# Kernel optimization log

Hardware: AMD Instinct MI355X
Metric: run time of the kernel (lower is better)

Reference implementation:

```python
import jax, jax.numpy as jnp
import numpy as np

LN_EPS = 1e-5  # torch.nn.LayerNorm default


def setup_inputs() -> dict:
    key = jax.random.key(0)
    k1, k2 = jax.random.split(key)
    C = 64
    x = jax.random.normal(k1, (1, C, 64, 96, 96), dtype=jnp.float32)
    ln_gamma = jnp.ones((C,), jnp.float32)
    ln_beta = jnp.zeros((C,), jnp.float32)
    # Conv3d(C, 3C, 1, groups=C) -> per-channel scalar weight [3C] and bias [3C]
    conv_w = jax.random.normal(k2, (3 * C,), dtype=jnp.float32) * 0.02
    conv_b = jnp.zeros((3 * C,), jnp.float32)
    return {"x": x, "ln_gamma": ln_gamma, "ln_beta": ln_beta,
            "conv_w": conv_w, "conv_b": conv_b}


def reference(x, ln_gamma, ln_beta, conv_w, conv_b):
    B, C, D, H, W = x.shape
    N = D * H * W
    xf = x.reshape(B, C, N)  # [B, C, N]

    # LayerNorm over the channel dim (module permutes channels last)
    mean = jnp.mean(xf, axis=1, keepdims=True)
    var = jnp.mean(jnp.square(xf - mean), axis=1, keepdims=True)
    y = (xf - mean) * jax.lax.rsqrt(var + LN_EPS)
    y = y * ln_gamma[None, :, None] + ln_beta[None, :, None]

    # grouped 1x1x1 conv: output channel o reads input channel o // 3
    idx = jnp.arange(3 * C) // 3
    y3 = y[:, idx, :] * conv_w[None, :, None] + conv_b[None, :, None]  # [B, 3C, N]
    q, k, v = jnp.split(y3, 3, axis=1)  # each [B, C, N]

    # channel (cross-covariance) attention: logits [B, C, C]
    logits = jnp.einsum('bcn,bkn->bck', q, k) * (C ** -0.5)
    attn = jax.nn.softmax(logits, axis=-1)  # max-subtraction built in
    out = jnp.einsum('bck,bkn->bcn', attn, v).reshape(B, C, D, H, W)
    return x + out
```

## Files before the change

kernel.cpp:

```cpp
#include <hip/hip_runtime.h>

#define NPOS 589824
#define LN_EPS 1e-5f

typedef _Float16 half8 __attribute__((ext_vector_type(8)));
typedef _Float16 half2_t __attribute__((ext_vector_type(2)));
typedef float f32x4 __attribute__((ext_vector_type(4)));
typedef float f32x2 __attribute__((ext_vector_type(2)));

static __device__ __forceinline__ half2_t pk16(float a, float b) {
    return __builtin_bit_cast(half2_t, __builtin_amdgcn_cvt_pkrtz(a, b));
}

#define KB_BLOCKS 1152
#define YSTR 520


__global__ __launch_bounds__(256) void csa_stats(
    const float* __restrict__ x, float* __restrict__ stats)
{
    const int g = blockIdx.x * 256 + threadIdx.x;
    const f32x4* __restrict__ x4 = (const f32x4*)x;
    f32x4 s = {0.f,0.f,0.f,0.f}, sq = s;
    #pragma unroll
    for (int c = 0; c < 64; ++c) {
        f32x4 v = x4[(size_t)c * (NPOS/4) + g];
        s += v;
        sq += v * v;
    }
    const f32x4 mu = s * (1.f/64.f);
    const f32x4 var = sq * (1.f/64.f) - mu * mu;
    f32x4 o0, o1;
    o0[0] = mu[0]; o0[2] = mu[1]; o1[0] = mu[2]; o1[2] = mu[3];
    o0[1] = rsqrtf(fmaxf(var[0], 0.f) + LN_EPS);
    o0[3] = rsqrtf(fmaxf(var[1], 0.f) + LN_EPS);
    o1[1] = rsqrtf(fmaxf(var[2], 0.f) + LN_EPS);
    o1[3] = rsqrtf(fmaxf(var[3], 0.f) + LN_EPS);
    f32x4* st4 = (f32x4*)stats;
    st4[2*g]     = o0;
    st4[2*g + 1] = o1;
}

__global__ __launch_bounds__(256, 3) void csa_gram(
    const float* __restrict__ x, const float* __restrict__ lng,
    const float* __restrict__ lnb, const float* __restrict__ stats,
    float* __restrict__ partials)
{
    __shared__ __align__(16) _Float16 Y[45][YSTR];
    const int tid = threadIdx.x;
    const int lane = tid & 63;
    const int wv = tid >> 6;

    for (int i = tid; i < YSTR; i += 256) {
        Y[43][i] = (_Float16)1.0f;
        Y[44][i] = (_Float16)0.0f;
    }

    const int t = blockIdx.x * 256 + tid;
    const f32x4 st = ((const f32x4*)stats)[t];
    const float mu0 = st[0], rin0 = st[1], mu1 = st[2], rin1 = st[3];
    const int n0 = t * 2;
    #pragma unroll
    for (int c = 0; c < 43; ++c) {
        f32x2 v = *(const f32x2*)(x + (size_t)c * NPOS + n0);
        const float g = lng[c], b = lnb[c];
        const float y0 = fmaf((v[0] - mu0) * rin0, g, b);
        const float y1 = fmaf((v[1] - mu1) * rin1, g, b);
        *(half2_t*)&Y[c][tid * 2] = pk16(y0, y1);
    }
    __syncthreads();

    f32x4 acc00 = {0.f,0.f,0.f,0.f}, acc01 = acc00, acc10 = acc00, acc11 = acc00;
    const int row = lane & 15;
    const int sub = (lane >> 4) & 3;
    const int kbase = wv * 128 + sub * 8;
    const int r16 = row + 16;
    const int ra1 = (r16 < 22) ? r16 : ((r16 == 22) ? 43 : 44);
    const int rb1 = (r16 < 22) ? (r16 + 21) : ((r16 == 22) ? 43 : 44);
    #pragma unroll
    for (int s2 = 0; s2 < 4; ++s2) {
        const int kk = kbase + s2 * 32;
        half8 a0 = *(const half8*)&Y[row][kk];
        half8 a1 = *(const half8*)&Y[ra1][kk];
        half8 b0 = *(const half8*)&Y[row + 21][kk];
        half8 b1 = *(const half8*)&Y[rb1][kk];
        acc00 = __builtin_amdgcn_mfma_f32_16x16x32_f16(a0, b0, acc00, 0, 0, 0);
        acc01 = __builtin_amdgcn_mfma_f32_16x16x32_f16(a0, b1, acc01, 0, 0, 0);
        acc10 = __builtin_amdgcn_mfma_f32_16x16x32_f16(a1, b0, acc10, 0, 0, 0);
        acc11 = __builtin_amdgcn_mfma_f32_16x16x32_f16(a1, b1, acc11, 0, 0, 0);
    }
    __syncthreads();

    float* G32 = (float*)&Y[0][0];
    for (int e = tid; e < 1024; e += 256) G32[e] = 0.f;
    __syncthreads();
    const int r0 = (lane >> 4) * 4, c0 = lane & 15;
    #pragma unroll
    for (int r = 0; r < 4; ++r) {
        atomicAdd(&G32[(r0 + r) * 32 + c0],            acc00[r]);
        atomicAdd(&G32[(r0 + r) * 32 + 16 + c0],       acc01[r]);
        atomicAdd(&G32[(16 + r0 + r) * 32 + c0],       acc10[r]);
        atomicAdd(&G32[(16 + r0 + r) * 32 + 16 + c0],  acc11[r]);
    }
    __syncthreads();
    for (int e = tid; e < 576; e += 256) {
        const int r = e / 24, c = e % 24;
        partials[(size_t)blockIdx.x * 576 + e] = G32[r * 32 + c];
    }
}

__global__ __launch_bounds__(256) void csa_k2(const float* __restrict__ partials,
                                              float* __restrict__ gfin)
{
    const int tid = threadIdx.x;
    const int e = blockIdx.x * 16 + (tid >> 4);
    const int g = tid & 15;
    float s = 0.f;
    for (int b = g; b < KB_BLOCKS; b += 16)
        s += partials[(size_t)b * 576 + e];
    s += __shfl_down(s, 8, 16);
    s += __shfl_down(s, 4, 16);
    s += __shfl_down(s, 2, 16);
    s += __shfl_down(s, 1, 16);
    if (g == 0) gfin[e] = s;
}

__global__ void csa_k3(const float* __restrict__ G, const float* __restrict__ cw,
                       const float* __restrict__ cb, float* __restrict__ M,
                       float* __restrict__ betaO)
{
    const int c = threadIdx.x;
    __shared__ float lg[64][65];
    const float wq = cw[c], bq = cb[c];
    const int a = c / 3;
    const float Sa = G[a * 24 + 22];
    float mx = -1e30f;
    #pragma unroll
    for (int k = 0; k < 64; ++k) {
        const float wk = cw[64 + k], bk = cb[64 + k];
        const int b = (64 + k) / 3 - 21;
        const float Gab = G[a * 24 + b];
        const float Sb  = G[22 * 24 + b];
        float lo = 0.125f * (wq * wk * Gab + wq * bk * Sa + bq * wk * Sb
                             + bq * bk * (float)NPOS);
        lg[c][k] = lo;
        mx = fmaxf(mx, lo);
    }
    float sum = 0.f;
    #pragma unroll
    for (int k = 0; k < 64; ++k) {
        float e = expf(lg[c][k] - mx);
        lg[c][k] = e; sum += e;
    }
    const float inv = 1.f / sum;
    float Ml[22];
    #pragma unroll
    for (int m = 0; m < 22; ++m) Ml[m] = 0.f;
    float bacc = 0.f;
    #pragma unroll
    for (int k = 0; k < 64; ++k) {
        const float attn = lg[c][k] * inv;
        const int mm = (128 + k) / 3 - 42;
        Ml[mm] = fmaf(attn, cw[128 + k], Ml[mm]);
        bacc   = fmaf(attn, cb[128 + k], bacc);
    }
    #pragma unroll
    for (int m = 0; m < 22; ++m) M[c * 22 + m] = Ml[m];
    betaO[c] = bacc;
}

__global__ __launch_bounds__(256, 2) void csa_k4(
    const float* __restrict__ x, const float* __restrict__ lng,
    const float* __restrict__ lnb, const float* __restrict__ M,
    const float* __restrict__ betaO, float* __restrict__ out)
{
    const int n0 = (blockIdx.x * 256 + threadIdx.x) * 2;
    f32x2 xv[64];
    f32x2 s = {0.f, 0.f}, sq = s;
    #pragma unroll
    for (int c = 0; c < 64; ++c) {
        f32x2 v = *(const f32x2*)(x + (size_t)c * NPOS + n0);
        xv[c] = v; s += v; sq += v * v;
    }
    const f32x2 mu = s * (1.f/64.f);
    const f32x2 var = sq * (1.f/64.f) - mu * mu;
    const float rin0 = rsqrtf(fmaxf(var[0], 0.f) + LN_EPS);
    const float rin1 = rsqrtf(fmaxf(var[1], 0.f) + LN_EPS);
    f32x2 y[22];
    #pragma unroll
    for (int m = 0; m < 22; ++m) {
        const float g = lng[42 + m], b = lnb[42 + m];
        y[m][0] = fmaf((xv[42 + m][0] - mu[0]) * rin0, g, b);
        y[m][1] = fmaf((xv[42 + m][1] - mu[1]) * rin1, g, b);
    }
    #pragma unroll
    for (int c = 0; c < 64; ++c) {
        const float bb = betaO[c];
        f32x2 a = {bb, bb};
        #pragma unroll
        for (int m = 0; m < 22; ++m) {
            const float w = M[c * 22 + m];
            a[0] = fmaf(w, y[m][0], a[0]);
            a[1] = fmaf(w, y[m][1], a[1]);
        }
        f32x2 o = xv[c] + a;
        __builtin_nontemporal_store(o, (f32x2*)(out + (size_t)c * NPOS + n0));
    }
}

extern "C" void kernel_launch(void* const* d_in, const int* in_sizes, int n_in,
                              void* d_out, int out_size, void* d_ws, size_t ws_size,
                              hipStream_t stream) {
    const float* x   = (const float*)d_in[0];
    const float* lng = (const float*)d_in[1];
    const float* lnb = (const float*)d_in[2];
    const float* cw  = (const float*)d_in[3];
    const float* cb  = (const float*)d_in[4];
    float* out = (float*)d_out;

    float* wsf   = (float*)d_ws;
    float* Gf    = wsf;
    float* Mf    = wsf + 1024;
    float* Bf    = wsf + 1024 + 64 * 22;
    float* stats = (float*)((char*)d_ws + 16384);
    float* Pf    = (float*)((char*)d_ws + 16384 + (size_t)NPOS * 8);

    hipLaunchKernelGGL(csa_stats, dim3(NPOS / 1024), dim3(256), 0, stream,
                       x, stats);
    hipLaunchKernelGGL(csa_gram, dim3(KB_BLOCKS), dim3(256), 0, stream,
                       x, lng, lnb, stats, Pf);
    hipLaunchKernelGGL(csa_k2, dim3(36), dim3(256), 0, stream, Pf, Gf);
    hipLaunchKernelGGL(csa_k3, dim3(1), dim3(64), 0, stream, Gf, cw, cb, Mf, Bf);
    hipLaunchKernelGGL(csa_k4, dim3(NPOS / 512), dim3(256), 0, stream,
                       x, lng, lnb, Mf, Bf, out);
}
```

Measured before the change: 167.4 us.

## Stream gram tiles via global_load_lds and reuse precomputed LN stats in output kernel

```diff
diff --git a/kernel.cpp b/kernel.cpp
--- a/kernel.cpp
+++ b/kernel.cpp
@@ -4,16 +4,13 @@
 #define LN_EPS 1e-5f
 
 typedef _Float16 half8 __attribute__((ext_vector_type(8)));
-typedef _Float16 half2_t __attribute__((ext_vector_type(2)));
 typedef float f32x4 __attribute__((ext_vector_type(4)));
 typedef float f32x2 __attribute__((ext_vector_type(2)));
 
-static __device__ __forceinline__ half2_t pk16(float a, float b) {
-    return __builtin_bit_cast(half2_t, __builtin_amdgcn_cvt_pkrtz(a, b));
-}
-
-#define KB_BLOCKS 1152
-#define YSTR 520
+#define GR_BLOCKS 1152
+#define TILE 128
+#define CPB 4
+#define YSTR 136
 
 
 __global__ __launch_bounds__(256) void csa_stats(
@@ -41,45 +38,55 @@
     st4[2*g + 1] = o1;
 }
 
-__global__ __launch_bounds__(256, 3) void csa_gram(
+__global__ __launch_bounds__(256, 4) void csa_gram(
     const float* __restrict__ x, const float* __restrict__ lng,
     const float* __restrict__ lnb, const float* __restrict__ stats,
     float* __restrict__ partials)
 {
+    __shared__ __align__(16) float XT[44][TILE];
     __shared__ __align__(16) _Float16 Y[45][YSTR];
     const int tid = threadIdx.x;
     const int lane = tid & 63;
     const int wv = tid >> 6;
+    const int p = tid & 127;
+    const int cbase = (tid >> 7) * 22;
 
     for (int i = tid; i < YSTR; i += 256) {
         Y[43][i] = (_Float16)1.0f;
         Y[44][i] = (_Float16)0.0f;
     }
 
-    const int t = blockIdx.x * 256 + tid;
-    const f32x4 st = ((const f32x4*)stats)[t];
-    const float mu0 = st[0], rin0 = st[1], mu1 = st[2], rin1 = st[3];
-    const int n0 = t * 2;
-    #pragma unroll
-    for (int c = 0; c < 43; ++c) {
-        f32x2 v = *(const f32x2*)(x + (size_t)c * NPOS + n0);
-        const float g = lng[c], b = lnb[c];
-        const float y0 = fmaf((v[0] - mu0) * rin0, g, b);
-        const float y1 = fmaf((v[1] - mu1) * rin1, g, b);
-        *(half2_t*)&Y[c][tid * 2] = pk16(y0, y1);
-    }
-    __syncthreads();
-
     f32x4 acc00 = {0.f,0.f,0.f,0.f}, acc01 = acc00, acc10 = acc00, acc11 = acc00;
     const int row = lane & 15;
     const int sub = (lane >> 4) & 3;
-    const int kbase = wv * 128 + sub * 8;
+    const int kk = wv * 32 + sub * 8;
     const int r16 = row + 16;
     const int ra1 = (r16 < 22) ? r16 : ((r16 == 22) ? 43 : 44);
     const int rb1 = (r16 < 22) ? (r16 + 21) : ((r16 == 22) ? 43 : 44);
-    #pragma unroll
-    for (int s2 = 0; s2 < 4; ++s2) {
-        const int kk = kbase + s2 * 32;
+    const int pos0 = blockIdx.x * (CPB * TILE);
+    const int rhalf = lane >> 5;
+    const int cq = lane & 31;
+
+    for (int ck = 0; ck < CPB; ++ck) {
+        const int n0 = pos0 + ck * TILE;
+        #pragma unroll
+        for (int j = 0; j < 6; ++j) {
+            const int i = wv * 6 + j;
+            if (i < 22) {
+                const float* g = x + (size_t)(2*i + rhalf) * NPOS + n0 + cq * 4;
+                __builtin_amdgcn_global_load_lds(g, &XT[2*i][0], 16, 0, 0);
+            }
+        }
+        __syncthreads();
+        const f32x2 st = ((const f32x2*)stats)[n0 + p];
+        const float mu = st[0], rin = st[1];
+        #pragma unroll
+        for (int k = 0; k < 22; ++k) {
+            const int c = cbase + k;
+            if (c < 43)
+                Y[c][p] = (_Float16)fmaf((XT[c][p] - mu) * rin, lng[c], lnb[c]);
+        }
+        __syncthreads();
         half8 a0 = *(const half8*)&Y[row][kk];
         half8 a1 = *(const half8*)&Y[ra1][kk];
         half8 b0 = *(const half8*)&Y[row + 21][kk];
@@ -88,19 +95,19 @@
         acc01 = __builtin_amdgcn_mfma_f32_16x16x32_f16(a0, b1, acc01, 0, 0, 0);
         acc10 = __builtin_amdgcn_mfma_f32_16x16x32_f16(a1, b0, acc10, 0, 0, 0);
         acc11 = __builtin_amdgcn_mfma_f32_16x16x32_f16(a1, b1, acc11, 0, 0, 0);
-    }
-    __syncthreads();
-
-    float* G32 = (float*)&Y[0][0];
+        __syncthreads();
+    }
+
+    float* G32 = (float*)&XT[0][0];
     for (int e = tid; e < 1024; e += 256) G32[e] = 0.f;
     __syncthreads();
-    const int r0 = (lane >> 4) * 4, c0 = lane & 15;
+    const int r0 = (lane >> 4) * 4, cc = lane & 15;
     #pragma unroll
     for (int r = 0; r < 4; ++r) {
-        atomicAdd(&G32[(r0 + r) * 32 + c0],            acc00[r]);
-        atomicAdd(&G32[(r0 + r) * 32 + 16 + c0],       acc01[r]);
-        atomicAdd(&G32[(16 + r0 + r) * 32 + c0],       acc10[r]);
-        atomicAdd(&G32[(16 + r0 + r) * 32 + 16 + c0],  acc11[r]);
+        atomicAdd(&G32[(r0 + r) * 32 + cc],            acc00[r]);
+        atomicAdd(&G32[(r0 + r) * 32 + 16 + cc],       acc01[r]);
+        atomicAdd(&G32[(16 + r0 + r) * 32 + cc],       acc10[r]);
+        atomicAdd(&G32[(16 + r0 + r) * 32 + 16 + cc],  acc11[r]);
     }
     __syncthreads();
     for (int e = tid; e < 576; e += 256) {
@@ -116,7 +123,7 @@
     const int e = blockIdx.x * 16 + (tid >> 4);
     const int g = tid & 15;
     float s = 0.f;
-    for (int b = g; b < KB_BLOCKS; b += 16)
+    for (int b = g; b < GR_BLOCKS; b += 16)
         s += partials[(size_t)b * 576 + e];
     s += __shfl_down(s, 8, 16);
     s += __shfl_down(s, 4, 16);
@@ -169,32 +176,27 @@
     betaO[c] = bacc;
 }
 
-__global__ __launch_bounds__(256, 2) void csa_k4(
+__global__ __launch_bounds__(256, 4) void csa_k4(
     const float* __restrict__ x, const float* __restrict__ lng,
-    const float* __restrict__ lnb, const float* __restrict__ M,
-    const float* __restrict__ betaO, float* __restrict__ out)
-{
-    const int n0 = (blockIdx.x * 256 + threadIdx.x) * 2;
-    f32x2 xv[64];
-    f32x2 s = {0.f, 0.f}, sq = s;
+    const float* __restrict__ lnb, const float* __restrict__ stats,
+    const float* __restrict__ M, const float* __restrict__ betaO,
+    float* __restrict__ out)
+{
+    const int gt = blockIdx.x * 256 + threadIdx.x;
+    const int n0 = gt * 2;
+    const f32x4 st = ((const f32x4*)stats)[gt];
+    const float mu0 = st[0], rin0 = st[1], mu1 = st[2], rin1 = st[3];
+    f32x2 y[22];
+    #pragma unroll
+    for (int m = 0; m < 22; ++m) {
+        f32x2 v = *(const f32x2*)(x + (size_t)(42 + m) * NPOS + n0);
+        const float g = lng[42 + m], b = lnb[42 + m];
+        y[m][0] = fmaf((v[0] - mu0) * rin0, g, b);
+        y[m][1] = fmaf((v[1] - mu1) * rin1, g, b);
+    }
     #pragma unroll
     for (int c = 0; c < 64; ++c) {
         f32x2 v = *(const f32x2*)(x + (size_t)c * NPOS + n0);
-        xv[c] = v; s += v; sq += v * v;
-    }
-    const f32x2 mu = s * (1.f/64.f);
-    const f32x2 var = sq * (1.f/64.f) - mu * mu;
-    const float rin0 = rsqrtf(fmaxf(var[0], 0.f) + LN_EPS);
-    const float rin1 = rsqrtf(fmaxf(var[1], 0.f) + LN_EPS);
-    f32x2 y[22];
-    #pragma unroll
-    for (int m = 0; m < 22; ++m) {
-        const float g = lng[42 + m], b = lnb[42 + m];
-        y[m][0] = fmaf((xv[42 + m][0] - mu[0]) * rin0, g, b);
-        y[m][1] = fmaf((xv[42 + m][1] - mu[1]) * rin1, g, b);
-    }
-    #pragma unroll
-    for (int c = 0; c < 64; ++c) {
         const float bb = betaO[c];
         f32x2 a = {bb, bb};
         #pragma unroll
@@ -203,7 +205,7 @@
             a[0] = fmaf(w, y[m][0], a[0]);
             a[1] = fmaf(w, y[m][1], a[1]);
         }
-        f32x2 o = xv[c] + a;
+        f32x2 o = v + a;
         __builtin_nontemporal_store(o, (f32x2*)(out + (size_t)c * NPOS + n0));
     }
 }
@@ -227,10 +229,10 @@
 
     hipLaunchKernelGGL(csa_stats, dim3(NPOS / 1024), dim3(256), 0, stream,
                        x, stats);
-    hipLaunchKernelGGL(csa_gram, dim3(KB_BLOCKS), dim3(256), 0, stream,
+    hipLaunchKernelGGL(csa_gram, dim3(GR_BLOCKS), dim3(256), 0, stream,
                        x, lng, lnb, stats, Pf);
     hipLaunchKernelGGL(csa_k2, dim3(36), dim3(256), 0, stream, Pf, Gf);
     hipLaunchKernelGGL(csa_k3, dim3(1), dim3(64), 0, stream, Gf, cw, cb, Mf, Bf);
     hipLaunchKernelGGL(csa_k4, dim3(NPOS / 512), dim3(256), 0, stream,
-                       x, lng, lnb, Mf, Bf, out);
-}
+                       x, lng, lnb, stats, Mf, Bf, out);
+}
```

Result: slower. 179.8 us (+7.4%).
